# Performance work log

Measured on AMD Instinct MI355X. Metric: run time of the kernel, lower is better.

The kernel has to match this reference:

```python
import jax, jax.numpy as jnp
import numpy as np

EPS = 1e-16
COS_EPS = 1e-8  # torch cosine_similarity clamp


def setup_inputs() -> dict:
    key = jax.random.key(0)
    ks = jax.random.split(key, 9)
    B, N, M = 128, 8192, 64
    return {
        "memory": jax.random.normal(ks[0], (B, N, M), dtype=jnp.float32),
        "k": jax.random.normal(ks[1], (B, M), dtype=jnp.float32),
        "beta": jax.random.uniform(ks[2], (B, 1), dtype=jnp.float32),
        "g": jax.random.uniform(ks[3], (B, 1), dtype=jnp.float32),
        "s": jax.random.uniform(ks[4], (B, 3), dtype=jnp.float32),
        "gamma": jax.random.uniform(ks[5], (B, 1), dtype=jnp.float32),
        "w_prev": jax.random.uniform(ks[6], (B, N), dtype=jnp.float32),
        "e": jax.random.uniform(ks[7], (B, M), dtype=jnp.float32),
        "a": jax.random.normal(ks[8], (B, M), dtype=jnp.float32),
    }


def reference(memory, k, beta, g, s, gamma, w_prev, e, a):
    # --- address (section 3.3) ---
    # content similarity: cosine(memory + eps, k + eps) along feature dim
    mem = memory + EPS                      # [B, N, M]
    kk = k[:, None, :] + EPS                # [B, 1, M]
    dot = jnp.sum(mem * kk, axis=-1)        # [B, N]
    denom = jnp.maximum(
        jnp.linalg.norm(mem, axis=-1) * jnp.linalg.norm(kk, axis=-1), COS_EPS
    )
    w_r = jax.nn.softmax(beta * (dot / denom), axis=1)   # [B, N]
    # interpolate with previous weighting
    w_g = g * w_r + (1.0 - g) * w_prev                   # [B, N]
    # circular shift: conv1d of [w[-1], w, w[0]] with 3-tap kernel s
    # c[i] = w[(i-1)%N]*s0 + w[i]*s1 + w[(i+1)%N]*s2
    shifted = (
        jnp.roll(w_g, 1, axis=1) * s[:, 0:1]
        + w_g * s[:, 1:2]
        + jnp.roll(w_g, -1, axis=1) * s[:, 2:3]
    )                                                     # [B, N]
    # sharpen: w**gamma, renormalize
    w_pow = shifted ** gamma
    w = w_pow / (jnp.sum(w_pow, axis=1, keepdims=True) + EPS)  # [B, N]

    # --- read (section 3.1) ---
    r = jnp.einsum("bn,bnm->bm", w, memory)               # [B, M]

    # --- write (section 3.2): erase then add (rank-1 outer products) ---
    erase = w[:, :, None] * e[:, None, :]                 # [B, N, M]
    add = w[:, :, None] * a[:, None, :]                   # [B, N, M]
    new_memory = memory * (1.0 - erase) + add             # [B, N, M]

    return w, r, new_memory
```

## Files before the change

### kernel.cpp

```cpp
#include <hip/hip_runtime.h>
#include <cmath>


namespace {
constexpr int B = 128;
constexpr int N = 8192;
constexpr int M = 64;
constexpr float F_EPS = 1e-16f;
constexpr float F_COS_EPS = 1e-8f;

constexpr int ROWS = 128;
constexpr int CHUNKS = N / ROWS;
constexpr int T2 = 1024;
constexpr int PER = N / T2;
}

typedef float vfloat4 __attribute__((ext_vector_type(4)));

__global__ __launch_bounds__(256) void score_kernel(
    const float* __restrict__ memory, const float* __restrict__ k,
    const float* __restrict__ beta, float* __restrict__ p_out,
    float* __restrict__ partial)
{
    const int b     = blockIdx.x / CHUNKS;
    const int chunk = blockIdx.x % CHUNKS;
    const int wave  = threadIdx.x >> 6;
    const int lane  = threadIdx.x & 63;
    const int grp   = lane >> 3;
    const int sub   = lane & 7;

    const float4* k4 = reinterpret_cast<const float4*>(k + (size_t)b * M);
    const float4 kva = k4[sub];
    const float4 kvb = k4[sub + 8];
    const float4 kea = make_float4(kva.x + F_EPS, kva.y + F_EPS,
                                   kva.z + F_EPS, kva.w + F_EPS);
    const float4 keb = make_float4(kvb.x + F_EPS, kvb.y + F_EPS,
                                   kvb.z + F_EPS, kvb.w + F_EPS);
    float kn2 = kea.x*kea.x + kea.y*kea.y + kea.z*kea.z + kea.w*kea.w
              + keb.x*keb.x + keb.y*keb.y + keb.z*keb.z + keb.w*keb.w;
    #pragma unroll
    for (int m = 1; m <= 4; m <<= 1) kn2 += __shfl_xor(kn2, m, 64);
    const float knorm = sqrtf(kn2);
    const float bb = beta[b];

    const int row0 = chunk * ROWS + wave * (ROWS / 4);

    float psum = 0.0f;

    #pragma unroll
    for (int it = 0; it < 4; ++it) {
        const int row = row0 + it * 8 + grp;
        const float4* m4p =
            reinterpret_cast<const float4*>(memory + ((size_t)b * N + row) * M);
        const float4 mva = m4p[sub];
        const float4 mvb = m4p[sub + 8];
        const float4 mea = make_float4(mva.x + F_EPS, mva.y + F_EPS,
                                       mva.z + F_EPS, mva.w + F_EPS);
        const float4 meb = make_float4(mvb.x + F_EPS, mvb.y + F_EPS,
                                       mvb.z + F_EPS, mvb.w + F_EPS);
        float dot = mea.x*kea.x + mea.y*kea.y + mea.z*kea.z + mea.w*kea.w
                  + meb.x*keb.x + meb.y*keb.y + meb.z*keb.z + meb.w*keb.w;
        float n2  = mea.x*mea.x + mea.y*mea.y + mea.z*mea.z + mea.w*mea.w
                  + meb.x*meb.x + meb.y*meb.y + meb.z*meb.z + meb.w*meb.w;
        #pragma unroll
        for (int m = 1; m <= 4; m <<= 1) {
            dot += __shfl_xor(dot, m, 64);
            n2  += __shfl_xor(n2,  m, 64);
        }
        if (sub == 0) {
            const float denom = fmaxf(sqrtf(n2) * knorm, F_COS_EPS);
            const float pe = expf(bb * (dot / denom));
            p_out[(size_t)b * N + row] = pe;
            psum += pe;
        }
    }

    psum += __shfl_xor(psum, 8, 64);
    psum += __shfl_xor(psum, 16, 64);
    psum += __shfl_xor(psum, 32, 64);

    __shared__ float ps[4];
    if (lane == 0) ps[wave] = psum;
    __syncthreads();
    if (threadIdx.x == 0)
        partial[b * CHUNKS + chunk] = ps[0] + ps[1] + ps[2] + ps[3];
}

__global__ __launch_bounds__(T2) void weight_kernel(
    const float* __restrict__ p, const float* __restrict__ g,
    const float* __restrict__ s, const float* __restrict__ gamma,
    const float* __restrict__ w_prev, float* __restrict__ w_out,
    float* __restrict__ r_out)
{
    const int b    = blockIdx.x;
    const int tid  = threadIdx.x;
    const int lane = tid & 63;
    const int wave = tid >> 6;

    __shared__ float wg[N];
    __shared__ float red[T2 / 64];
    __shared__ float sS;

    float pv_r[PER], wp_r[PER];
    #pragma unroll
    for (int i = 0; i < PER; i++) {
        const int idx = tid + i * T2;
        pv_r[i] = p[(size_t)b * N + idx];
        wp_r[i] = w_prev[(size_t)b * N + idx];
    }

    if (tid < 64) {
        float v = r_out[(size_t)b * M + tid];
        #pragma unroll
        for (int m = 1; m <= 32; m <<= 1) v += __shfl_xor(v, m, 64);
        if (tid == 0) sS = v;
    }
    __syncthreads();
    const float invS = 1.0f / sS;

    if (tid < M) r_out[(size_t)b * M + tid] = 0.0f;

    const float gb  = g[b];
    const float gS  = gb * invS;
    const float gmb = 1.0f - gb;
    #pragma unroll
    for (int i = 0; i < PER; i++) {
        const int idx = tid + i * T2;
        wg[idx] = gS * pv_r[i] + gmb * wp_r[i];
    }
    __syncthreads();

    const float s0 = s[b * 3 + 0], s1 = s[b * 3 + 1], s2 = s[b * 3 + 2];
    const float gm = gamma[b];
    float pv[PER];
    float lsum = 0.0f;
    #pragma unroll
    for (int i = 0; i < PER; i++) {
        const int idx = tid + i * T2;
        const float sh = wg[(idx - 1) & (N - 1)] * s0
                       + wg[idx] * s1
                       + wg[(idx + 1) & (N - 1)] * s2;
        pv[i] = powf(sh, gm);
        lsum += pv[i];
    }
    #pragma unroll
    for (int m = 1; m <= 32; m <<= 1) lsum += __shfl_xor(lsum, m, 64);
    if (lane == 0) red[wave] = lsum;
    __syncthreads();
    float bsum = 0.0f;
    #pragma unroll
    for (int i = 0; i < T2 / 64; i++) bsum += red[i];
    const float invn = 1.0f / (bsum + F_EPS);

    #pragma unroll
    for (int i = 0; i < PER; i++) {
        const int idx = tid + i * T2;
        w_out[(size_t)b * N + idx] = pv[i] * invn;
    }
}

__global__ __launch_bounds__(256) void update_kernel(
    const float* __restrict__ memory, const float* __restrict__ e,
    const float* __restrict__ a, const float* __restrict__ w,
    float* __restrict__ newmem, float* __restrict__ r_out)
{
    const int b     = blockIdx.x / CHUNKS;
    const int chunk = blockIdx.x % CHUNKS;
    const int wave  = threadIdx.x >> 6;
    const int lane  = threadIdx.x & 63;
    const int grp   = lane >> 3;
    const int sub   = lane & 7;

    const float4* e4 = reinterpret_cast<const float4*>(e + (size_t)b * M);
    const float4* a4 = reinterpret_cast<const float4*>(a + (size_t)b * M);
    const float4 eva = e4[sub], evb = e4[sub + 8];
    const float4 ava = a4[sub], avb = a4[sub + 8];

    const int row0 = chunk * ROWS + wave * (ROWS / 4);

    float4 accA = make_float4(0.f, 0.f, 0.f, 0.f);
    float4 accB = make_float4(0.f, 0.f, 0.f, 0.f);

    #pragma unroll
    for (int it = 0; it < 4; ++it) {
        const int row = row0 + it * 8 + grp;
        const size_t off = ((size_t)b * N + row) * M;
        const float4* m4p = reinterpret_cast<const float4*>(memory + off);
        const float4 mva = m4p[sub];
        const float4 mvb = m4p[sub + 8];
        const float ww = w[(size_t)b * N + row];

        vfloat4 nva, nvb;
        nva.x = mva.x * (1.0f - ww * eva.x) + ww * ava.x;
        nva.y = mva.y * (1.0f - ww * eva.y) + ww * ava.y;
        nva.z = mva.z * (1.0f - ww * eva.z) + ww * ava.z;
        nva.w = mva.w * (1.0f - ww * eva.w) + ww * ava.w;
        nvb.x = mvb.x * (1.0f - ww * evb.x) + ww * avb.x;
        nvb.y = mvb.y * (1.0f - ww * evb.y) + ww * avb.y;
        nvb.z = mvb.z * (1.0f - ww * evb.z) + ww * avb.z;
        nvb.w = mvb.w * (1.0f - ww * evb.w) + ww * avb.w;
        __builtin_nontemporal_store(nva, (vfloat4*)(newmem + off) + sub);
        __builtin_nontemporal_store(nvb, (vfloat4*)(newmem + off) + sub + 8);

        accA.x += ww * mva.x;  accA.y += ww * mva.y;
        accA.z += ww * mva.z;  accA.w += ww * mva.w;
        accB.x += ww * mvb.x;  accB.y += ww * mvb.y;
        accB.z += ww * mvb.z;  accB.w += ww * mvb.w;
    }

    #pragma unroll
    for (int m = 8; m <= 32; m <<= 1) {
        accA.x += __shfl_xor(accA.x, m, 64);
        accA.y += __shfl_xor(accA.y, m, 64);
        accA.z += __shfl_xor(accA.z, m, 64);
        accA.w += __shfl_xor(accA.w, m, 64);
        accB.x += __shfl_xor(accB.x, m, 64);
        accB.y += __shfl_xor(accB.y, m, 64);
        accB.z += __shfl_xor(accB.z, m, 64);
        accB.w += __shfl_xor(accB.w, m, 64);
    }

    __shared__ float sred[4][M];
    if (grp == 0) {
        sred[wave][sub * 4 + 0] = accA.x;
        sred[wave][sub * 4 + 1] = accA.y;
        sred[wave][sub * 4 + 2] = accA.z;
        sred[wave][sub * 4 + 3] = accA.w;
        sred[wave][32 + sub * 4 + 0] = accB.x;
        sred[wave][32 + sub * 4 + 1] = accB.y;
        sred[wave][32 + sub * 4 + 2] = accB.z;
        sred[wave][32 + sub * 4 + 3] = accB.w;
    }
    __syncthreads();
    if (threadIdx.x < M) {
        const float v = sred[0][threadIdx.x] + sred[1][threadIdx.x]
                      + sred[2][threadIdx.x] + sred[3][threadIdx.x];
        atomicAdd(&r_out[(size_t)b * M + threadIdx.x], v);
    }
}

extern "C" void kernel_launch(void* const* d_in, const int* in_sizes, int n_in,
                              void* d_out, int out_size, void* d_ws, size_t ws_size,
                              hipStream_t stream) {
    const float* memory = (const float*)d_in[0];
    const float* k      = (const float*)d_in[1];
    const float* beta   = (const float*)d_in[2];
    const float* g      = (const float*)d_in[3];
    const float* s      = (const float*)d_in[4];
    const float* gamma  = (const float*)d_in[5];
    const float* w_prev = (const float*)d_in[6];
    const float* e      = (const float*)d_in[7];
    const float* a      = (const float*)d_in[8];

    float* out    = (float*)d_out;
    float* w_out  = out;
    float* r_out  = out + (size_t)B * N;
    float* newmem = out + (size_t)B * N + (size_t)B * M;

    float* p       = newmem;
    float* partsum = r_out;

    const dim3 blk(256);
    const dim3 grid1(B * CHUNKS);

    score_kernel<<<grid1, blk, 0, stream>>>(memory, k, beta, p, partsum);
    weight_kernel<<<dim3(B), dim3(T2), 0, stream>>>(p, g, s, gamma,
                                                    w_prev, w_out, r_out);
    update_kernel<<<grid1, blk, 0, stream>>>(memory, e, a, w_out,
                                             newmem, r_out);
}
```

Before: 507.5 us.

## Fuse score, weight, and update kernels into one cooperative persistent kernel

Result: slower. 643.3 us (+26.8%).

```diff
diff --git a/kernel.cpp b/kernel.cpp
--- a/kernel.cpp
+++ b/kernel.cpp
@@ -1,5 +1,8 @@
 #include <hip/hip_runtime.h>
+#include <hip/hip_cooperative_groups.h>
 #include <cmath>
+
+namespace cg = cooperative_groups;
 
 
 namespace {
@@ -10,232 +13,244 @@
 constexpr float F_COS_EPS = 1e-8f;
 
 constexpr int ROWS = 128;
-constexpr int CHUNKS = N / ROWS;
-constexpr int T2 = 1024;
-constexpr int PER = N / T2;
+constexpr int NCHUNK = B * (N / ROWS);
+constexpr int SEGROWS = 1024;
+constexpr int SEG_PER_B = N / SEGROWS;
+constexpr int NSEG = B * SEG_PER_B;
 }
 
 typedef float vfloat4 __attribute__((ext_vector_type(4)));
 
-__global__ __launch_bounds__(256) void score_kernel(
+__device__ float g_part_s[NCHUNK];
+__device__ float g_part_t[NSEG];
+
+__global__ __launch_bounds__(256, 4) void fused_kernel(
     const float* __restrict__ memory, const float* __restrict__ k,
-    const float* __restrict__ beta, float* __restrict__ p_out,
-    float* __restrict__ partial)
+    const float* __restrict__ beta, const float* __restrict__ g,
+    const float* __restrict__ s, const float* __restrict__ gamma,
+    const float* __restrict__ w_prev, const float* __restrict__ e,
+    const float* __restrict__ a, float* __restrict__ w_out,
+    float* __restrict__ r_out, float* __restrict__ newmem)
 {
-    const int b     = blockIdx.x / CHUNKS;
-    const int chunk = blockIdx.x % CHUNKS;
-    const int wave  = threadIdx.x >> 6;
-    const int lane  = threadIdx.x & 63;
-    const int grp   = lane >> 3;
-    const int sub   = lane & 7;
-
-    const float4* k4 = reinterpret_cast<const float4*>(k + (size_t)b * M);
-    const float4 kva = k4[sub];
-    const float4 kvb = k4[sub + 8];
-    const float4 kea = make_float4(kva.x + F_EPS, kva.y + F_EPS,
-                                   kva.z + F_EPS, kva.w + F_EPS);
-    const float4 keb = make_float4(kvb.x + F_EPS, kvb.y + F_EPS,
-                                   kvb.z + F_EPS, kvb.w + F_EPS);
-    float kn2 = kea.x*kea.x + kea.y*kea.y + kea.z*kea.z + kea.w*kea.w
-              + keb.x*keb.x + keb.y*keb.y + keb.z*keb.z + keb.w*keb.w;
-    #pragma unroll
-    for (int m = 1; m <= 4; m <<= 1) kn2 += __shfl_xor(kn2, m, 64);
-    const float knorm = sqrtf(kn2);
-    const float bb = beta[b];
-
-    const int row0 = chunk * ROWS + wave * (ROWS / 4);
-
-    float psum = 0.0f;
-
-    #pragma unroll
-    for (int it = 0; it < 4; ++it) {
-        const int row = row0 + it * 8 + grp;
-        const float4* m4p =
-            reinterpret_cast<const float4*>(memory + ((size_t)b * N + row) * M);
-        const float4 mva = m4p[sub];
-        const float4 mvb = m4p[sub + 8];
-        const float4 mea = make_float4(mva.x + F_EPS, mva.y + F_EPS,
-                                       mva.z + F_EPS, mva.w + F_EPS);
-        const float4 meb = make_float4(mvb.x + F_EPS, mvb.y + F_EPS,
-                                       mvb.z + F_EPS, mvb.w + F_EPS);
-        float dot = mea.x*kea.x + mea.y*kea.y + mea.z*kea.z + mea.w*kea.w
-                  + meb.x*keb.x + meb.y*keb.y + meb.z*keb.z + meb.w*keb.w;
-        float n2  = mea.x*mea.x + mea.y*mea.y + mea.z*mea.z + mea.w*mea.w
-                  + meb.x*meb.x + meb.y*meb.y + meb.z*meb.z + meb.w*meb.w;
-        #pragma unroll
-        for (int m = 1; m <= 4; m <<= 1) {
-            dot += __shfl_xor(dot, m, 64);
-            n2  += __shfl_xor(n2,  m, 64);
-        }
-        if (sub == 0) {
-            const float denom = fmaxf(sqrtf(n2) * knorm, F_COS_EPS);
-            const float pe = expf(bb * (dot / denom));
-            p_out[(size_t)b * N + row] = pe;
-            psum += pe;
-        }
-    }
-
-    psum += __shfl_xor(psum, 8, 64);
-    psum += __shfl_xor(psum, 16, 64);
-    psum += __shfl_xor(psum, 32, 64);
-
-    __shared__ float ps[4];
-    if (lane == 0) ps[wave] = psum;
-    __syncthreads();
-    if (threadIdx.x == 0)
-        partial[b * CHUNKS + chunk] = ps[0] + ps[1] + ps[2] + ps[3];
-}
-
-__global__ __launch_bounds__(T2) void weight_kernel(
-    const float* __restrict__ p, const float* __restrict__ g,
-    const float* __restrict__ s, const float* __restrict__ gamma,
-    const float* __restrict__ w_prev, float* __restrict__ w_out,
-    float* __restrict__ r_out)
-{
-    const int b    = blockIdx.x;
     const int tid  = threadIdx.x;
+    const int wave = tid >> 6;
     const int lane = tid & 63;
-    const int wave = tid >> 6;
-
-    __shared__ float wg[N];
-    __shared__ float red[T2 / 64];
-    __shared__ float sS;
-
-    float pv_r[PER], wp_r[PER];
-    #pragma unroll
-    for (int i = 0; i < PER; i++) {
-        const int idx = tid + i * T2;
-        pv_r[i] = p[(size_t)b * N + idx];
-        wp_r[i] = w_prev[(size_t)b * N + idx];
-    }
-
-    if (tid < 64) {
-        float v = r_out[(size_t)b * M + tid];
-        #pragma unroll
-        for (int m = 1; m <= 32; m <<= 1) v += __shfl_xor(v, m, 64);
-        if (tid == 0) sS = v;
-    }
-    __syncthreads();
-    const float invS = 1.0f / sS;
-
-    if (tid < M) r_out[(size_t)b * M + tid] = 0.0f;
-
-    const float gb  = g[b];
-    const float gS  = gb * invS;
-    const float gmb = 1.0f - gb;
-    #pragma unroll
-    for (int i = 0; i < PER; i++) {
-        const int idx = tid + i * T2;
-        wg[idx] = gS * pv_r[i] + gmb * wp_r[i];
-    }
-    __syncthreads();
-
-    const float s0 = s[b * 3 + 0], s1 = s[b * 3 + 1], s2 = s[b * 3 + 2];
-    const float gm = gamma[b];
-    float pv[PER];
-    float lsum = 0.0f;
-    #pragma unroll
-    for (int i = 0; i < PER; i++) {
-        const int idx = tid + i * T2;
-        const float sh = wg[(idx - 1) & (N - 1)] * s0
-                       + wg[idx] * s1
-                       + wg[(idx + 1) & (N - 1)] * s2;
-        pv[i] = powf(sh, gm);
-        lsum += pv[i];
-    }
-    #pragma unroll
-    for (int m = 1; m <= 32; m <<= 1) lsum += __shfl_xor(lsum, m, 64);
-    if (lane == 0) red[wave] = lsum;
-    __syncthreads();
-    float bsum = 0.0f;
-    #pragma unroll
-    for (int i = 0; i < T2 / 64; i++) bsum += red[i];
-    const float invn = 1.0f / (bsum + F_EPS);
-
-    #pragma unroll
-    for (int i = 0; i < PER; i++) {
-        const int idx = tid + i * T2;
-        w_out[(size_t)b * N + idx] = pv[i] * invn;
-    }
-}
-
-__global__ __launch_bounds__(256) void update_kernel(
-    const float* __restrict__ memory, const float* __restrict__ e,
-    const float* __restrict__ a, const float* __restrict__ w,
-    float* __restrict__ newmem, float* __restrict__ r_out)
-{
-    const int b     = blockIdx.x / CHUNKS;
-    const int chunk = blockIdx.x % CHUNKS;
-    const int wave  = threadIdx.x >> 6;
-    const int lane  = threadIdx.x & 63;
-    const int grp   = lane >> 3;
-    const int sub   = lane & 7;
-
-    const float4* e4 = reinterpret_cast<const float4*>(e + (size_t)b * M);
-    const float4* a4 = reinterpret_cast<const float4*>(a + (size_t)b * M);
-    const float4 eva = e4[sub], evb = e4[sub + 8];
-    const float4 ava = a4[sub], avb = a4[sub + 8];
-
-    const int row0 = chunk * ROWS + wave * (ROWS / 4);
-
-    float4 accA = make_float4(0.f, 0.f, 0.f, 0.f);
-    float4 accB = make_float4(0.f, 0.f, 0.f, 0.f);
-
-    #pragma unroll
-    for (int it = 0; it < 4; ++it) {
-        const int row = row0 + it * 8 + grp;
-        const size_t off = ((size_t)b * N + row) * M;
-        const float4* m4p = reinterpret_cast<const float4*>(memory + off);
-        const float4 mva = m4p[sub];
-        const float4 mvb = m4p[sub + 8];
-        const float ww = w[(size_t)b * N + row];
-
-        vfloat4 nva, nvb;
-        nva.x = mva.x * (1.0f - ww * eva.x) + ww * ava.x;
-        nva.y = mva.y * (1.0f - ww * eva.y) + ww * ava.y;
-        nva.z = mva.z * (1.0f - ww * eva.z) + ww * ava.z;
-        nva.w = mva.w * (1.0f - ww * eva.w) + ww * ava.w;
-        nvb.x = mvb.x * (1.0f - ww * evb.x) + ww * avb.x;
-        nvb.y = mvb.y * (1.0f - ww * evb.y) + ww * avb.y;
-        nvb.z = mvb.z * (1.0f - ww * evb.z) + ww * avb.z;
-        nvb.w = mvb.w * (1.0f - ww * evb.w) + ww * avb.w;
-        __builtin_nontemporal_store(nva, (vfloat4*)(newmem + off) + sub);
-        __builtin_nontemporal_store(nvb, (vfloat4*)(newmem + off) + sub + 8);
-
-        accA.x += ww * mva.x;  accA.y += ww * mva.y;
-        accA.z += ww * mva.z;  accA.w += ww * mva.w;
-        accB.x += ww * mvb.x;  accB.y += ww * mvb.y;
-        accB.z += ww * mvb.z;  accB.w += ww * mvb.w;
-    }
-
-    #pragma unroll
-    for (int m = 8; m <= 32; m <<= 1) {
-        accA.x += __shfl_xor(accA.x, m, 64);
-        accA.y += __shfl_xor(accA.y, m, 64);
-        accA.z += __shfl_xor(accA.z, m, 64);
-        accA.w += __shfl_xor(accA.w, m, 64);
-        accB.x += __shfl_xor(accB.x, m, 64);
-        accB.y += __shfl_xor(accB.y, m, 64);
-        accB.z += __shfl_xor(accB.z, m, 64);
-        accB.w += __shfl_xor(accB.w, m, 64);
-    }
-
-    __shared__ float sred[4][M];
-    if (grp == 0) {
-        sred[wave][sub * 4 + 0] = accA.x;
-        sred[wave][sub * 4 + 1] = accA.y;
-        sred[wave][sub * 4 + 2] = accA.z;
-        sred[wave][sub * 4 + 3] = accA.w;
-        sred[wave][32 + sub * 4 + 0] = accB.x;
-        sred[wave][32 + sub * 4 + 1] = accB.y;
-        sred[wave][32 + sub * 4 + 2] = accB.z;
-        sred[wave][32 + sub * 4 + 3] = accB.w;
-    }
-    __syncthreads();
-    if (threadIdx.x < M) {
-        const float v = sred[0][threadIdx.x] + sred[1][threadIdx.x]
-                      + sred[2][threadIdx.x] + sred[3][threadIdx.x];
-        atomicAdd(&r_out[(size_t)b * M + threadIdx.x], v);
+    const int grp  = lane >> 3;
+    const int sub  = lane & 7;
+    const int G    = gridDim.x;
+
+    float* const p = newmem;
+
+    __shared__ float lds_red[16];
+    __shared__ float lds_wg[SEGROWS + 2];
+    __shared__ float lds_w[SEGROWS];
+    __shared__ float lds_sred[4][M];
+    __shared__ float lds_bcast[2];
+
+    for (int u = blockIdx.x; u < NCHUNK; u += G) {
+        const int b     = u >> 6;
+        const int chunk = u & 63;
+
+        if (u < (B * M) / 256) r_out[u * 256 + tid] = 0.0f;
+
+        const float4* k4 = reinterpret_cast<const float4*>(k + (size_t)b * M);
+        const float4 kva = k4[sub];
+        const float4 kvb = k4[sub + 8];
+        const float4 kea = make_float4(kva.x + F_EPS, kva.y + F_EPS,
+                                       kva.z + F_EPS, kva.w + F_EPS);
+        const float4 keb = make_float4(kvb.x + F_EPS, kvb.y + F_EPS,
+                                       kvb.z + F_EPS, kvb.w + F_EPS);
+        float kn2 = kea.x*kea.x + kea.y*kea.y + kea.z*kea.z + kea.w*kea.w
+                  + keb.x*keb.x + keb.y*keb.y + keb.z*keb.z + keb.w*keb.w;
+        #pragma unroll
+        for (int m = 1; m <= 4; m <<= 1) kn2 += __shfl_xor(kn2, m, 64);
+        const float knorm = sqrtf(kn2);
+        const float bb = beta[b];
+
+        const int row0 = chunk * ROWS + wave * 32;
+        float psum = 0.0f;
+
+        #pragma unroll
+        for (int it = 0; it < 4; ++it) {
+            const int row = row0 + it * 8 + grp;
+            const float4* m4p = reinterpret_cast<const float4*>(
+                memory + ((size_t)b * N + row) * M);
+            const float4 mva = m4p[sub];
+            const float4 mvb = m4p[sub + 8];
+            const float4 mea = make_float4(mva.x + F_EPS, mva.y + F_EPS,
+                                           mva.z + F_EPS, mva.w + F_EPS);
+            const float4 meb = make_float4(mvb.x + F_EPS, mvb.y + F_EPS,
+                                           mvb.z + F_EPS, mvb.w + F_EPS);
+            float dot = mea.x*kea.x + mea.y*kea.y + mea.z*kea.z + mea.w*kea.w
+                      + meb.x*keb.x + meb.y*keb.y + meb.z*keb.z + meb.w*keb.w;
+            float n2  = mea.x*mea.x + mea.y*mea.y + mea.z*mea.z + mea.w*mea.w
+                      + meb.x*meb.x + meb.y*meb.y + meb.z*meb.z + meb.w*meb.w;
+            #pragma unroll
+            for (int m = 1; m <= 4; m <<= 1) {
+                dot += __shfl_xor(dot, m, 64);
+                n2  += __shfl_xor(n2,  m, 64);
+            }
+            if (sub == 0) {
+                const float denom = fmaxf(sqrtf(n2) * knorm, F_COS_EPS);
+                const float pe = expf(bb * (dot / denom));
+                p[(size_t)b * N + row] = pe;
+                psum += pe;
+            }
+        }
+
+        psum += __shfl_xor(psum, 8, 64);
+        psum += __shfl_xor(psum, 16, 64);
+        psum += __shfl_xor(psum, 32, 64);
+        if (lane == 0) lds_red[wave] = psum;
+        __syncthreads();
+        if (tid == 0)
+            g_part_s[u] = lds_red[0] + lds_red[1] + lds_red[2] + lds_red[3];
+        __syncthreads();
+    }
+
+    cg::this_grid().sync();
+
+    for (int u = blockIdx.x; u < NSEG; u += G) {
+        const int b  = u >> 3;
+        const int n0 = (u & 7) * SEGROWS;
+
+        if (tid < 64) {
+            float v = g_part_s[b * 64 + tid];
+            #pragma unroll
+            for (int m = 1; m <= 32; m <<= 1) v += __shfl_xor(v, m, 64);
+            if (tid == 0) lds_bcast[0] = v;
+        }
+        __syncthreads();
+        const float invS = 1.0f / lds_bcast[0];
+        const float gb  = g[b];
+        const float gS  = gb * invS;
+        const float gmb = 1.0f - gb;
+
+        #pragma unroll
+        for (int j = 0; j < 4; j++) {
+            const int loc = tid + j * 256;
+            const int idx = b * N + n0 + loc;
+            lds_wg[loc + 1] = gS * p[idx] + gmb * w_prev[idx];
+        }
+        if (tid == 0) {
+            const int prev = (n0 - 1) & (N - 1);
+            const int next = (n0 + SEGROWS) & (N - 1);
+            lds_wg[0] = gS * p[b * N + prev] + gmb * w_prev[b * N + prev];
+            lds_wg[SEGROWS + 1] =
+                gS * p[b * N + next] + gmb * w_prev[b * N + next];
+        }
+        __syncthreads();
+
+        const float s0 = s[b*3+0], s1 = s[b*3+1], s2 = s[b*3+2];
+        const float gm = gamma[b];
+        float lsum = 0.0f;
+        #pragma unroll
+        for (int j = 0; j < 4; j++) {
+            const int loc = tid + j * 256;
+            const float sh = lds_wg[loc] * s0 + lds_wg[loc + 1] * s1
+                           + lds_wg[loc + 2] * s2;
+            const float pv = powf(sh, gm);
+            w_out[b * N + n0 + loc] = pv;
+            lsum += pv;
+        }
+        #pragma unroll
+        for (int m = 1; m <= 32; m <<= 1) lsum += __shfl_xor(lsum, m, 64);
+        if (lane == 0) lds_red[wave] = lsum;
+        __syncthreads();
+        if (tid == 0)
+            g_part_t[u] = lds_red[0] + lds_red[1] + lds_red[2] + lds_red[3];
+        __syncthreads();
+    }
+
+    cg::this_grid().sync();
+
+    for (int u = blockIdx.x; u < NSEG; u += G) {
+        const int b  = u >> 3;
+        const int n0 = (u & 7) * SEGROWS;
+
+        if (tid == 0) {
+            float t = 0.0f;
+            #pragma unroll
+            for (int i = 0; i < SEG_PER_B; i++) t += g_part_t[b * SEG_PER_B + i];
+            lds_bcast[1] = 1.0f / (t + F_EPS);
+        }
+        __syncthreads();
+        const float invn = lds_bcast[1];
+
+        #pragma unroll
+        for (int j = 0; j < 4; j++) {
+            const int loc = tid + j * 256;
+            const float w = w_out[b * N + n0 + loc] * invn;
+            w_out[b * N + n0 + loc] = w;
+            lds_w[loc] = w;
+        }
+        __syncthreads();
+
+        const float4* e4 = reinterpret_cast<const float4*>(e + (size_t)b * M);
+        const float4* a4 = reinterpret_cast<const float4*>(a + (size_t)b * M);
+        const float4 eva = e4[sub], evb = e4[sub + 8];
+        const float4 ava = a4[sub], avb = a4[sub + 8];
+
+        float4 accA = make_float4(0.f, 0.f, 0.f, 0.f);
+        float4 accB = make_float4(0.f, 0.f, 0.f, 0.f);
+        const int rbase = n0 + wave * 256;
+
+        #pragma unroll 4
+        for (int it = 0; it < 32; ++it) {
+            const int row = rbase + it * 8 + grp;
+            const size_t off = ((size_t)b * N + row) * M;
+            const float4* m4p = reinterpret_cast<const float4*>(memory + off);
+            const float4 mva = m4p[sub];
+            const float4 mvb = m4p[sub + 8];
+            const float ww = lds_w[row - n0];
+
+            vfloat4 nva, nvb;
+            nva.x = mva.x * (1.0f - ww * eva.x) + ww * ava.x;
+            nva.y = mva.y * (1.0f - ww * eva.y) + ww * ava.y;
+            nva.z = mva.z * (1.0f - ww * eva.z) + ww * ava.z;
+            nva.w = mva.w * (1.0f - ww * eva.w) + ww * ava.w;
+            nvb.x = mvb.x * (1.0f - ww * evb.x) + ww * avb.x;
+            nvb.y = mvb.y * (1.0f - ww * evb.y) + ww * avb.y;
+            nvb.z = mvb.z * (1.0f - ww * evb.z) + ww * avb.z;
+            nvb.w = mvb.w * (1.0f - ww * evb.w) + ww * avb.w;
+            __builtin_nontemporal_store(nva, (vfloat4*)(newmem + off) + sub);
+            __builtin_nontemporal_store(nvb, (vfloat4*)(newmem + off) + sub + 8);
+
+            accA.x += ww * mva.x;  accA.y += ww * mva.y;
+            accA.z += ww * mva.z;  accA.w += ww * mva.w;
+            accB.x += ww * mvb.x;  accB.y += ww * mvb.y;
+            accB.z += ww * mvb.z;  accB.w += ww * mvb.w;
+        }
+
+        #pragma unroll
+        for (int m = 8; m <= 32; m <<= 1) {
+            accA.x += __shfl_xor(accA.x, m, 64);
+            accA.y += __shfl_xor(accA.y, m, 64);
+            accA.z += __shfl_xor(accA.z, m, 64);
+            accA.w += __shfl_xor(accA.w, m, 64);
+            accB.x += __shfl_xor(accB.x, m, 64);
+            accB.y += __shfl_xor(accB.y, m, 64);
+            accB.z += __shfl_xor(accB.z, m, 64);
+            accB.w += __shfl_xor(accB.w, m, 64);
+        }
+
+        if (grp == 0) {
+            lds_sred[wave][sub * 4 + 0] = accA.x;
+            lds_sred[wave][sub * 4 + 1] = accA.y;
+            lds_sred[wave][sub * 4 + 2] = accA.z;
+            lds_sred[wave][sub * 4 + 3] = accA.w;
+            lds_sred[wave][32 + sub * 4 + 0] = accB.x;
+            lds_sred[wave][32 + sub * 4 + 1] = accB.y;
+            lds_sred[wave][32 + sub * 4 + 2] = accB.z;
+            lds_sred[wave][32 + sub * 4 + 3] = accB.w;
+        }
+        __syncthreads();
+        if (tid < M) {
+            const float v = lds_sred[0][tid] + lds_sred[1][tid]
+                          + lds_sred[2][tid] + lds_sred[3][tid];
+            atomicAdd(&r_out[(size_t)b * M + tid], v);
+        }
+        __syncthreads();
     }
 }
 
@@ -257,15 +272,26 @@
     float* r_out  = out + (size_t)B * N;
     float* newmem = out + (size_t)B * N + (size_t)B * M;
 
-    float* p       = newmem;
-    float* partsum = r_out;
-
-    const dim3 blk(256);
-    const dim3 grid1(B * CHUNKS);
-
-    score_kernel<<<grid1, blk, 0, stream>>>(memory, k, beta, p, partsum);
-    weight_kernel<<<dim3(B), dim3(T2), 0, stream>>>(p, g, s, gamma,
-                                                    w_prev, w_out, r_out);
-    update_kernel<<<grid1, blk, 0, stream>>>(memory, e, a, w_out,
-                                             newmem, r_out);
+    static int s_grid = 0;
+    if (s_grid == 0) {
+        int dev = 0;
+        hipGetDevice(&dev);
+        int cus = 0;
+        hipDeviceGetAttribute(&cus, hipDeviceAttributeMultiprocessorCount, dev);
+        int maxb = 0;
+        hipOccupancyMaxActiveBlocksPerMultiprocessor(
+            &maxb, (const void*)fused_kernel, 256, 0);
+        long gg = (long)(cus > 0 ? cus : 256) * (maxb > 0 ? maxb : 1);
+        if (gg > 2048) gg = 2048;
+        if (gg < 1) gg = 1;
+        s_grid = (int)gg;
+    }
+
+    void* args[12] = {
+        (void*)&memory, (void*)&k, (void*)&beta, (void*)&g, (void*)&s,
+        (void*)&gamma, (void*)&w_prev, (void*)&e, (void*)&a,
+        (void*)&w_out, (void*)&r_out, (void*)&newmem
+    };
+    hipLaunchCooperativeKernel((const void*)fused_kernel, dim3(s_grid),
+                               dim3(256), args, 0, stream);
 }
```

## Use one thread per row in score kernel and double rows per block

Applied to the files above, without the earlier changes.

Result: no change. 510.1 us (+0.5%).

```diff
diff --git a/kernel.cpp b/kernel.cpp
--- a/kernel.cpp
+++ b/kernel.cpp
@@ -9,8 +9,10 @@
 constexpr float F_EPS = 1e-16f;
 constexpr float F_COS_EPS = 1e-8f;
 
-constexpr int ROWS = 128;
-constexpr int CHUNKS = N / ROWS;
+constexpr int SROWS = 256;
+constexpr int SCHUNKS = N / SROWS;
+constexpr int UROWS = 256;
+constexpr int UCHUNKS = N / UROWS;
 constexpr int T2 = 1024;
 constexpr int PER = N / T2;
 }
@@ -22,68 +24,46 @@
     const float* __restrict__ beta, float* __restrict__ p_out,
     float* __restrict__ partial)
 {
-    const int b     = blockIdx.x / CHUNKS;
-    const int chunk = blockIdx.x % CHUNKS;
-    const int wave  = threadIdx.x >> 6;
-    const int lane  = threadIdx.x & 63;
-    const int grp   = lane >> 3;
-    const int sub   = lane & 7;
-
-    const float4* k4 = reinterpret_cast<const float4*>(k + (size_t)b * M);
-    const float4 kva = k4[sub];
-    const float4 kvb = k4[sub + 8];
-    const float4 kea = make_float4(kva.x + F_EPS, kva.y + F_EPS,
-                                   kva.z + F_EPS, kva.w + F_EPS);
-    const float4 keb = make_float4(kvb.x + F_EPS, kvb.y + F_EPS,
-                                   kvb.z + F_EPS, kvb.w + F_EPS);
-    float kn2 = kea.x*kea.x + kea.y*kea.y + kea.z*kea.z + kea.w*kea.w
-              + keb.x*keb.x + keb.y*keb.y + keb.z*keb.z + keb.w*keb.w;
-    #pragma unroll
-    for (int m = 1; m <= 4; m <<= 1) kn2 += __shfl_xor(kn2, m, 64);
-    const float knorm = sqrtf(kn2);
-    const float bb = beta[b];
-
-    const int row0 = chunk * ROWS + wave * (ROWS / 4);
-
-    float psum = 0.0f;
-
-    #pragma unroll
-    for (int it = 0; it < 4; ++it) {
-        const int row = row0 + it * 8 + grp;
-        const float4* m4p =
-            reinterpret_cast<const float4*>(memory + ((size_t)b * N + row) * M);
-        const float4 mva = m4p[sub];
-        const float4 mvb = m4p[sub + 8];
-        const float4 mea = make_float4(mva.x + F_EPS, mva.y + F_EPS,
-                                       mva.z + F_EPS, mva.w + F_EPS);
-        const float4 meb = make_float4(mvb.x + F_EPS, mvb.y + F_EPS,
-                                       mvb.z + F_EPS, mvb.w + F_EPS);
-        float dot = mea.x*kea.x + mea.y*kea.y + mea.z*kea.z + mea.w*kea.w
-                  + meb.x*keb.x + meb.y*keb.y + meb.z*keb.z + meb.w*keb.w;
-        float n2  = mea.x*mea.x + mea.y*mea.y + mea.z*mea.z + mea.w*mea.w
-                  + meb.x*meb.x + meb.y*meb.y + meb.z*meb.z + meb.w*meb.w;
-        #pragma unroll
-        for (int m = 1; m <= 4; m <<= 1) {
-            dot += __shfl_xor(dot, m, 64);
-            n2  += __shfl_xor(n2,  m, 64);
-        }
-        if (sub == 0) {
-            const float denom = fmaxf(sqrtf(n2) * knorm, F_COS_EPS);
-            const float pe = expf(bb * (dot / denom));
-            p_out[(size_t)b * N + row] = pe;
-            psum += pe;
-        }
-    }
-
-    psum += __shfl_xor(psum, 8, 64);
-    psum += __shfl_xor(psum, 16, 64);
-    psum += __shfl_xor(psum, 32, 64);
-
-    __shared__ float ps[4];
-    if (lane == 0) ps[wave] = psum;
-    __syncthreads();
-    if (threadIdx.x == 0)
-        partial[b * CHUNKS + chunk] = ps[0] + ps[1] + ps[2] + ps[3];
+    const int b     = blockIdx.x >> 5;
+    const int chunk = blockIdx.x & (SCHUNKS - 1);
+    const int tid   = threadIdx.x;
+    const int lane  = tid & 63;
+    const int wave  = tid >> 6;
+
+    __shared__ float kl[M];
+    __shared__ float red[4];
+
+    if (tid < M) kl[tid] = k[(size_t)b * M + tid] + F_EPS;
+    __syncthreads();
+
+    const int row = chunk * SROWS + tid;
+    const float4* mrow =
+        reinterpret_cast<const float4*>(memory + ((size_t)b * N + row) * M);
+    const float4* k4 = reinterpret_cast<const float4*>(kl);
+
+    float dot = 0.f, n2 = 0.f, kn2 = 0.f;
+    #pragma unroll
+    for (int j = 0; j < M / 4; ++j) {
+        const float4 mv = mrow[j];
+        const float4 kv = k4[j];
+        const float mx = mv.x + F_EPS, my = mv.y + F_EPS,
+                    mz = mv.z + F_EPS, mw = mv.w + F_EPS;
+        dot += mx*kv.x + my*kv.y + mz*kv.z + mw*kv.w;
+        n2  += mx*mx + my*my + mz*mz + mw*mw;
+        kn2 += kv.x*kv.x + kv.y*kv.y + kv.z*kv.z + kv.w*kv.w;
+    }
+
+    const float denom = fmaxf(sqrtf(n2) * sqrtf(kn2), F_COS_EPS);
+    const float pe = expf(beta[b] * (dot / denom));
+    p_out[(size_t)b * N + row] = pe;
+
+    float psum = pe;
+    #pragma unroll
+    for (int m = 1; m <= 32; m <<= 1) psum += __shfl_xor(psum, m, 64);
+    if (lane == 0) red[wave] = psum;
+    __syncthreads();
+    if (tid == 0)
+        partial[(size_t)b * M + chunk] = red[0] + red[1] + red[2] + red[3];
 }
 
 __global__ __launch_bounds__(T2) void weight_kernel(
@@ -109,10 +89,10 @@
         wp_r[i] = w_prev[(size_t)b * N + idx];
     }
 
-    if (tid < 64) {
+    if (tid < 32) {
         float v = r_out[(size_t)b * M + tid];
         #pragma unroll
-        for (int m = 1; m <= 32; m <<= 1) v += __shfl_xor(v, m, 64);
+        for (int m = 1; m <= 16; m <<= 1) v += __shfl_xor(v, m, 64);
         if (tid == 0) sS = v;
     }
     __syncthreads();
@@ -164,8 +144,8 @@
     const float* __restrict__ a, const float* __restrict__ w,
     float* __restrict__ newmem, float* __restrict__ r_out)
 {
-    const int b     = blockIdx.x / CHUNKS;
-    const int chunk = blockIdx.x % CHUNKS;
+    const int b     = blockIdx.x >> 5;
+    const int chunk = blockIdx.x & (UCHUNKS - 1);
     const int wave  = threadIdx.x >> 6;
     const int lane  = threadIdx.x & 63;
     const int grp   = lane >> 3;
@@ -176,13 +156,13 @@
     const float4 eva = e4[sub], evb = e4[sub + 8];
     const float4 ava = a4[sub], avb = a4[sub + 8];
 
-    const int row0 = chunk * ROWS + wave * (ROWS / 4);
+    const int row0 = chunk * UROWS + wave * (UROWS / 4);
 
     float4 accA = make_float4(0.f, 0.f, 0.f, 0.f);
     float4 accB = make_float4(0.f, 0.f, 0.f, 0.f);
 
     #pragma unroll
-    for (int it = 0; it < 4; ++it) {
+    for (int it = 0; it < 8; ++it) {
         const int row = row0 + it * 8 + grp;
         const size_t off = ((size_t)b * N + row) * M;
         const float4* m4p = reinterpret_cast<const float4*>(memory + off);
@@ -260,12 +240,10 @@
     float* p       = newmem;
     float* partsum = r_out;
 
-    const dim3 blk(256);
-    const dim3 grid1(B * CHUNKS);
-
-    score_kernel<<<grid1, blk, 0, stream>>>(memory, k, beta, p, partsum);
+    score_kernel<<<dim3(B * SCHUNKS), dim3(256), 0, stream>>>(
+        memory, k, beta, p, partsum);
     weight_kernel<<<dim3(B), dim3(T2), 0, stream>>>(p, g, s, gamma,
                                                     w_prev, w_out, r_out);
-    update_kernel<<<grid1, blk, 0, stream>>>(memory, e, a, w_out,
-                                             newmem, r_out);
-}
+    update_kernel<<<dim3(B * UCHUNKS), dim3(256), 0, stream>>>(
+        memory, e, a, w_out, newmem, r_out);
+}
```
